# Optimization experiments

Hardware: AMD Instinct MI355X
Metric: run time of the kernel (lower is better)

## Reference

```python
import jax, jax.numpy as jnp
import numpy as np

D_MODEL = 1024
NUM_HEADS = 16
HEAD_DIM = D_MODEL // NUM_HEADS  # 64
ROPE_BASE = 10000.0


def _rope_tables(n_pos, dim):
    # 1D rotary tables for `dim` channels (rotate-half convention).
    inv_freq = 1.0 / (ROPE_BASE ** (jnp.arange(0, dim, 2, dtype=jnp.float32) / dim))
    ang = jnp.arange(n_pos, dtype=jnp.float32)[:, None] * inv_freq[None, :]  # (P, dim/2)
    cos = jnp.concatenate([jnp.cos(ang), jnp.cos(ang)], axis=-1)  # (P, dim)
    sin = jnp.concatenate([jnp.sin(ang), jnp.sin(ang)], axis=-1)
    return cos, sin


def _rotate_half(v):
    v1, v2 = jnp.split(v, 2, axis=-1)
    return jnp.concatenate([-v2, v1], axis=-1)


def rope_2d(x, H, W):
    # x: (N, H, W, nh, hd). First half of hd rotated by row index, second by col index.
    d_half = HEAD_DIM // 2
    x_h, x_w = x[..., :d_half], x[..., d_half:]
    cos_h, sin_h = _rope_tables(H, d_half)  # (H, d_half)
    cos_w, sin_w = _rope_tables(W, d_half)  # (W, d_half)
    cos_h = cos_h[None, :, None, None, :]
    sin_h = sin_h[None, :, None, None, :]
    cos_w = cos_w[None, None, :, None, :]
    sin_w = sin_w[None, None, :, None, :]
    x_h = x_h * cos_h + _rotate_half(x_h) * sin_h
    x_w = x_w * cos_w + _rotate_half(x_w) * sin_w
    return jnp.concatenate([x_h, x_w], axis=-1)


def setup_inputs() -> dict:
    key = jax.random.key(0)
    k_x, k_qkv, k_p, k_b = jax.random.split(key, 4)
    B, T, H, W = 4, 32, 16, 16
    x = jax.random.normal(k_x, (B, T, H, W, D_MODEL), dtype=jnp.float32)
    w_qkv = jax.random.normal(k_qkv, (D_MODEL, 3 * D_MODEL), dtype=jnp.float32) * 0.02
    w_proj = jax.random.normal(k_p, (D_MODEL, D_MODEL), dtype=jnp.float32) * 0.02
    b_proj = jax.random.normal(k_b, (D_MODEL,), dtype=jnp.float32) * 0.02
    return {"x": x, "w_qkv": w_qkv, "w_proj": w_proj, "b_proj": b_proj}


def reference(x, w_qkv, w_proj, b_proj):
    B, T, H, W, C = x.shape
    N, S = B * T, H * W
    scale = HEAD_DIM ** -0.5
    xf = x.reshape(N, S, C)
    qkv = xf @ w_qkv  # (N, S, 3C)  [qkv_bias=False]
    q, k, v = jnp.split(qkv, 3, axis=-1)
    q = q.reshape(N, H, W, NUM_HEADS, HEAD_DIM)
    k = k.reshape(N, H, W, NUM_HEADS, HEAD_DIM)
    v = v.reshape(N, S, NUM_HEADS, HEAD_DIM)
    q = rope_2d(q, H, W).reshape(N, S, NUM_HEADS, HEAD_DIM)
    k = rope_2d(k, H, W).reshape(N, S, NUM_HEADS, HEAD_DIM)
    attn = jnp.einsum('nshd,nthd->nhst', q, k) * scale  # (N, nh, S, S)
    attn = jax.nn.softmax(attn, axis=-1)  # attn_drop=0.0
    out = jnp.einsum('nhst,nthd->nshd', attn, v).reshape(N, S, C)
    out = out @ w_proj + b_proj
    return out.reshape(B, T, H, W, C)
```

## Files before the change

### kernel.cpp

```cpp
#include <hip/hip_runtime.h>
#include <hip/hip_bf16.h>
#include <stdint.h>

typedef __attribute__((ext_vector_type(8))) short bf16x8;
typedef __attribute__((ext_vector_type(4))) float f32x4;
typedef __attribute__((ext_vector_type(4))) unsigned short ushort4_t;

__device__ __forceinline__ unsigned short f2bf(float f) {
  union { float f; unsigned int i; } x; x.f = f;
  return (unsigned short)((x.i + 0x7fffu + ((x.i >> 16) & 1u)) >> 16);
}

__device__ __forceinline__ void gl_lds16(const void* g, void* l) {
  __builtin_amdgcn_global_load_lds(
      (const __attribute__((address_space(1))) unsigned int*)(uintptr_t)g,
      (__attribute__((address_space(3))) unsigned int*)(uint32_t)(uintptr_t)l,
      16, 0, 0);
}

__device__ __forceinline__ void bar() {
  asm volatile("" ::: "memory");
  __builtin_amdgcn_s_barrier();
  asm volatile("" ::: "memory");
}

__constant__ float INVF[16] = {
  1.0f,   0.56234132519f,  0.31622776601f,  0.17782794100f,
  0.1f,   0.056234132519f, 0.031622776601f, 0.017782794100f,
  0.01f,  0.0056234132519f,0.0031622776601f,0.0017782794100f,
  0.001f, 0.00056234132519f,0.00031622776601f,0.00017782794100f
};

__global__ __launch_bounds__(256) void k_conv_x(const float4* __restrict__ src,
                                                ushort4_t* __restrict__ dst, int n4) {
  int i = blockIdx.x * 256 + threadIdx.x;
  if (i < n4) {
    float4 v = src[i];
    ushort4_t r = { f2bf(v.x), f2bf(v.y), f2bf(v.z), f2bf(v.w) };
    dst[i] = r;
  }
}

__global__ __launch_bounds__(256) void k_transpose_bf16(const float* __restrict__ src,
                                                        unsigned short* __restrict__ dst,
                                                        int R, int C) {
  __shared__ unsigned short tile[64][65];
  const int bj = blockIdx.x, bi = blockIdx.y;
  const int t = threadIdx.x, lr = t >> 6, lc = t & 63;
  #pragma unroll
  for (int i = 0; i < 16; i++) {
    int r = i * 4 + lr;
    tile[r][lc] = f2bf(src[(size_t)(bi * 64 + r) * C + bj * 64 + lc]);
  }
  __syncthreads();
  #pragma unroll
  for (int i = 0; i < 16; i++) {
    int r = i * 4 + lr;
    dst[(size_t)(bj * 64 + r) * R + bi * 64 + lc] = tile[lc][r];
  }
}

template<int F32OUT, int ROPE>
__global__ __launch_bounds__(512, 1) void k_gemm_bt(
    const unsigned short* __restrict__ A, const unsigned short* __restrict__ B,
    unsigned short* __restrict__ Cb, float* __restrict__ Cf,
    const float* __restrict__ bias, int M, int N, int K) {
  __shared__ __align__(16) unsigned short As[3 * 256 * 64];
  __shared__ __align__(16) unsigned short Bs[3 * 128 * 64];
  const int tid = threadIdx.x;
  const int lane = tid & 63, wid = tid >> 6;
  const int cl = lane & 15, gr = lane >> 4;
  const int wm = wid >> 1, wn = wid & 1;
  const int l8 = lane >> 3, l7 = lane & 7;
  const int mBase = blockIdx.y * 256, nBase = blockIdx.x * 128;
  const int KT = K >> 6;
  const int ldsW = (wid * 8) * 64;

  const unsigned short* aP[4];
  const unsigned short* bP[2];
  #pragma unroll
  for (int i = 0; i < 4; i++)
    aP[i] = A + (size_t)(mBase + i * 64 + wid * 8 + l8) * K + (l7 ^ l8) * 8;
  #pragma unroll
  for (int i = 0; i < 2; i++)
    bP[i] = B + (size_t)(nBase + i * 64 + wid * 8 + l8) * K + (l7 ^ l8) * 8;

  const f32x4 zero4 = {0.f, 0.f, 0.f, 0.f};
  f32x4 acc[4][4];
  #pragma unroll
  for (int a = 0; a < 4; a++)
    #pragma unroll
    for (int b = 0; b < 4; b++) acc[a][b] = zero4;

  #pragma unroll
  for (int i = 0; i < 4; i++) gl_lds16(aP[i], &As[(i * 64) * 64 + ldsW]);
  #pragma unroll
  for (int i = 0; i < 2; i++) gl_lds16(bP[i], &Bs[(i * 64) * 64 + ldsW]);
  #pragma unroll
  for (int i = 0; i < 4; i++) gl_lds16(aP[i] + 64, &As[16384 + (i * 64) * 64 + ldsW]);
  #pragma unroll
  for (int i = 0; i < 2; i++) gl_lds16(bP[i] + 64, &Bs[8192 + (i * 64) * 64 + ldsW]);
  asm volatile("s_waitcnt vmcnt(6)" ::: "memory");
  bar();

  for (int c = 0; c < KT; ++c) {
    const int s = c % 3;
    const int sn = (c + 2) % 3;
    const unsigned short* as_ = As + s * 16384;
    const unsigned short* bs_ = Bs + s * 8192;
    const bool pf = (c + 2 < KT);

    #pragma unroll
    for (int kc = 0; kc < 2; ++kc) {
      bf16x8 af[4], bfv[4];
      const int coff = ((kc * 4 + gr) ^ (cl & 7)) * 8;
      #pragma unroll
      for (int t = 0; t < 4; t++) {
        af[t]  = *(const bf16x8*)&as_[(wm * 64 + t * 16 + cl) * 64 + coff];
        bfv[t] = *(const bf16x8*)&bs_[(wn * 64 + t * 16 + cl) * 64 + coff];
      }
      if (pf) {
        const int koff = (c + 2) * 64;
        if (kc == 0) {
          gl_lds16(aP[0] + koff, &As[sn * 16384 + (0 * 64) * 64 + ldsW]);
          gl_lds16(aP[1] + koff, &As[sn * 16384 + (1 * 64) * 64 + ldsW]);
          gl_lds16(aP[2] + koff, &As[sn * 16384 + (2 * 64) * 64 + ldsW]);
        } else {
          gl_lds16(aP[3] + koff, &As[sn * 16384 + (3 * 64) * 64 + ldsW]);
          gl_lds16(bP[0] + koff, &Bs[sn * 8192 + (0 * 64) * 64 + ldsW]);
          gl_lds16(bP[1] + koff, &Bs[sn * 8192 + (1 * 64) * 64 + ldsW]);
        }
      }
      bar();
      asm volatile("s_waitcnt lgkmcnt(0)" ::: "memory");
      __builtin_amdgcn_s_setprio(1);
      #pragma unroll
      for (int mt = 0; mt < 4; mt++)
        #pragma unroll
        for (int nt = 0; nt < 4; nt++)
          acc[mt][nt] = __builtin_amdgcn_mfma_f32_16x16x32_bf16(af[mt], bfv[nt], acc[mt][nt], 0, 0, 0);
      __builtin_amdgcn_s_setprio(0);
      if (kc == 0) {
        bar();
      } else {
        if (c + 2 < KT)      asm volatile("s_waitcnt vmcnt(6)" ::: "memory");
        else if (c + 1 < KT) asm volatile("s_waitcnt vmcnt(0)" ::: "memory");
        if (c + 1 < KT) bar();
      }
    }
  }

  if (ROPE && nBase < 2048) {
    const float f = INVF[cl];
    #pragma unroll
    for (int mt = 0; mt < 4; mt++)
      #pragma unroll
      for (int r = 0; r < 4; r++) {
        const int sp = (mBase + wm * 64 + mt * 16 + gr * 4 + r) & 255;
        float sh, ch, sw, cw;
        __sincosf((float)(sp >> 4) * f, &sh, &ch);
        __sincosf((float)(sp & 15) * f, &sw, &cw);
        const float a = acc[mt][0][r], b = acc[mt][1][r];
        const float cc = acc[mt][2][r], d = acc[mt][3][r];
        acc[mt][0][r] = a * ch - b * sh;
        acc[mt][1][r] = b * ch + a * sh;
        acc[mt][2][r] = cc * cw - d * sw;
        acc[mt][3][r] = d * cw + cc * sw;
      }
  }

  #pragma unroll
  for (int mt = 0; mt < 4; mt++)
    #pragma unroll
    for (int nt = 0; nt < 4; nt++)
      #pragma unroll
      for (int r = 0; r < 4; r++) {
        const int row = mBase + wm * 64 + mt * 16 + gr * 4 + r;
        const int col = nBase + wn * 64 + nt * 16 + cl;
        const float v = acc[mt][nt][r];
        if (F32OUT) Cf[(size_t)row * N + col] = v + bias[col];
        else        Cb[(size_t)row * N + col] = f2bf(v);
      }
}

__global__ __launch_bounds__(256, 3) void k_attn(const unsigned short* __restrict__ qkv,
                                                 unsigned short* __restrict__ attn_out) {
  __shared__ __align__(16) unsigned short Qp[4][64 * 64];
  __shared__ __align__(16) unsigned short Kt[64 * 64];
  __shared__ __align__(16) unsigned short Vt[64 * 64];
  const int blk = blockIdx.x;
  const int n = blk >> 4, h = blk & 15;
  const int tid = threadIdx.x;
  const int lane = tid & 63, wid = tid >> 6;
  const int cl = lane & 15, gr = lane >> 4;
  const int l8 = lane >> 3, l7 = lane & 7;
  const unsigned short* qbase = qkv + (size_t)n * 256 * 3072 + h * 64;
  const unsigned short* kbase = qbase + 1024;
  const unsigned short* vbase = qbase + 2048;

  #pragma unroll
  for (int i = 0; i < 8; i++)
    gl_lds16(qbase + (size_t)(wid * 64 + i * 8 + l8) * 3072 + (l7 ^ l8) * 8,
             &Qp[wid][i * 8 * 64]);
  #pragma unroll
  for (int i = 0; i < 2; i++) {
    const int r0 = (wid * 2 + i) * 8;
    gl_lds16(kbase + (size_t)(r0 + l8) * 3072 + (l7 ^ l8) * 8, &Kt[r0 * 64]);
  }

  unsigned int vr[2][4];
  #pragma unroll
  for (int i = 0; i < 2; i++) {
    const int u = i * 256 + tid;
    const int t0 = u >> 5, d = (u & 31) * 2;
    #pragma unroll
    for (int k = 0; k < 4; k++)
      vr[i][k] = *(const unsigned int*)(vbase + (size_t)(t0 + 16 * k) * 3072 + d);
  }
  __syncthreads();

  bf16x8 qf[4][2];
  #pragma unroll
  for (int mt = 0; mt < 4; mt++)
    #pragma unroll
    for (int kc = 0; kc < 2; kc++)
      qf[mt][kc] = *(const bf16x8*)&Qp[wid][(mt * 16 + cl) * 64 + ((kc * 4 + gr) ^ (cl & 7)) * 8];

  const f32x4 zero4 = {0.f, 0.f, 0.f, 0.f};
  f32x4 o[4][4];
  float lsum[4][4];
  #pragma unroll
  for (int a = 0; a < 4; a++)
    #pragma unroll
    for (int b = 0; b < 4; b++) { o[a][b] = zero4; lsum[a][b] = 0.f; }

  for (int tc = 0; tc < 4; tc++) {
    #pragma unroll
    for (int i = 0; i < 2; i++) {
      const int u = i * 256 + tid;
      const int t0 = u >> 5, d = (u & 31) * 2;
      const unsigned int r0 = vr[i][0], r1 = vr[i][1], r2 = vr[i][2], r3 = vr[i][3];
      uint2 lo, hi;
      lo.x = (r0 & 0xffffu) | (r1 << 16);
      lo.y = (r2 & 0xffffu) | (r3 << 16);
      hi.x = (r0 >> 16) | (r1 & 0xffff0000u);
      hi.y = (r2 >> 16) | (r3 & 0xffff0000u);
      *(uint2*)&Vt[d * 64 + ((t0 >> 1) ^ (d & 7)) * 8 + (t0 & 1) * 4] = lo;
      const int d1 = d + 1;
      *(uint2*)&Vt[d1 * 64 + ((t0 >> 1) ^ (d1 & 7)) * 8 + (t0 & 1) * 4] = hi;
    }
    if (tc < 3) {
      #pragma unroll
      for (int i = 0; i < 2; i++) {
        const int u = i * 256 + tid;
        const int t0 = u >> 5, d = (u & 31) * 2;
        #pragma unroll
        for (int k = 0; k < 4; k++)
          vr[i][k] = *(const unsigned int*)(vbase + (size_t)((tc + 1) * 64 + t0 + 16 * k) * 3072 + d);
      }
    }

    #pragma unroll
    for (int mt = 0; mt < 4; mt++) {
      f32x4 sacc[4] = {zero4, zero4, zero4, zero4};
      #pragma unroll
      for (int kc = 0; kc < 2; kc++)
        #pragma unroll
        for (int nt = 0; nt < 4; nt++) {
          const bf16x8 kf = *(const bf16x8*)&Kt[(nt * 16 + cl) * 64 + ((kc * 4 + gr) ^ (cl & 7)) * 8];
          sacc[nt] = __builtin_amdgcn_mfma_f32_16x16x32_bf16(qf[mt][kc], kf, sacc[nt], 0, 0, 0);
        }
      #pragma unroll
      for (int r = 0; r < 4; r++) {
        const float p0 = __expf(sacc[0][r] * 0.125f);
        const float p1 = __expf(sacc[1][r] * 0.125f);
        const float p2 = __expf(sacc[2][r] * 0.125f);
        const float p3 = __expf(sacc[3][r] * 0.125f);
        lsum[mt][r] += (p0 + p1) + (p2 + p3);
        float2 f01; f01.x = p0; f01.y = p1;
        float2 f23; f23.x = p2; f23.y = p3;
        __hip_bfloat162 b01 = __float22bfloat162_rn(f01);
        __hip_bfloat162 b23 = __float22bfloat162_rn(f23);
        union { __hip_bfloat162 h; unsigned int u; } c0, c1;
        c0.h = b01; c1.h = b23;
        uint2 w; w.x = c0.u; w.y = c1.u;
        const int m = mt * 16 + gr * 4 + r;
        *(uint2*)&Qp[wid][m * 64 + ((cl >> 1) ^ (m & 7)) * 8 + (cl & 1) * 4] = w;
      }
    }
    __syncthreads();

    if (tc < 3) {
      #pragma unroll
      for (int i = 0; i < 2; i++) {
        const int r0 = (wid * 2 + i) * 8;
        gl_lds16(kbase + (size_t)((tc + 1) * 64 + r0 + l8) * 3072 + (l7 ^ l8) * 8, &Kt[r0 * 64]);
      }
    }

    #pragma unroll
    for (int kc = 0; kc < 2; kc++) {
      bf16x8 vf[4], pf[4];
      #pragma unroll
      for (int dt = 0; dt < 4; dt++)
        vf[dt] = *(const bf16x8*)&Vt[(dt * 16 + cl) * 64 + ((kc * 4 + gr) ^ (cl & 7)) * 8];
      #pragma unroll
      for (int mt = 0; mt < 4; mt++)
        pf[mt] = *(const bf16x8*)&Qp[wid][(mt * 16 + cl) * 64 + ((kc * 4 + gr) ^ (cl & 7)) * 8];
      #pragma unroll
      for (int mt = 0; mt < 4; mt++)
        #pragma unroll
        for (int dt = 0; dt < 4; dt++)
          o[mt][dt] = __builtin_amdgcn_mfma_f32_16x16x32_bf16(pf[mt], vf[dt], o[mt][dt], 0, 0, 0);
    }
    __syncthreads();
  }

  #pragma unroll
  for (int mt = 0; mt < 4; mt++)
    #pragma unroll
    for (int r = 0; r < 4; r++) {
      float l = lsum[mt][r];
      l += __shfl_xor(l, 1);
      l += __shfl_xor(l, 2);
      l += __shfl_xor(l, 4);
      l += __shfl_xor(l, 8);
      const float inv = 1.0f / l;
      const int srow = wid * 64 + mt * 16 + gr * 4 + r;
      #pragma unroll
      for (int dt = 0; dt < 4; dt++)
        attn_out[(size_t)(n * 256 + srow) * 1024 + h * 64 + dt * 16 + cl] =
            f2bf(o[mt][dt][r] * inv);
    }
}

extern "C" void kernel_launch(void* const* d_in, const int* in_sizes, int n_in,
                              void* d_out, int out_size, void* d_ws, size_t ws_size,
                              hipStream_t stream) {
  const float* x      = (const float*)d_in[0];
  const float* w_qkv  = (const float*)d_in[1];
  const float* w_proj = (const float*)d_in[2];
  const float* b_proj = (const float*)d_in[3];
  float* out = (float*)d_out;
  char* ws = (char*)d_ws;

  unsigned short* x_bf    = (unsigned short*)ws;
  unsigned short* wqkvT   = (unsigned short*)(ws + 67108864);
  unsigned short* wprojT  = (unsigned short*)(ws + 73400320);
  unsigned short* qkvb    = (unsigned short*)(ws + 75497472);
  unsigned short* attn_bf = x_bf;

  k_conv_x<<<32768, 256, 0, stream>>>((const float4*)x, (ushort4_t*)x_bf, 8388608);
  k_transpose_bf16<<<dim3(48, 16), 256, 0, stream>>>(w_qkv, wqkvT, 1024, 3072);
  k_transpose_bf16<<<dim3(16, 16), 256, 0, stream>>>(w_proj, wprojT, 1024, 1024);

  k_gemm_bt<0, 1><<<dim3(24, 128), 512, 0, stream>>>(x_bf, wqkvT, qkvb, nullptr, nullptr,
                                                     32768, 3072, 1024);
  k_attn<<<2048, 256, 0, stream>>>(qkvb, attn_bf);

  k_gemm_bt<1, 0><<<dim3(8, 128), 512, 0, stream>>>(attn_bf, wprojT, nullptr, out, b_proj,
                                                    32768, 1024, 1024);
}
```

Before: 710.0 us.

## Enlarge GEMM tile to 256x256 with double-buffered LDS and 2 blocks/CU

The bf16 GEMM tile grows from 256x128 to 256x256, with a 2x4 warp grid and each warp computing 128x64 (8x4 MFMA tiles). The triple-buffered split prefetch becomes double buffering, where the whole next K-slice is issued at the top of each iteration and waited on once at the end. Launch bounds now ask for 2 blocks per CU. The aim is more arithmetic per LDS/global byte and fewer barriers per K-step. In exchange, the accumulator register count doubles, which may conflict with the 2-block occupancy hint or cause spills, and prefetch overlap is shallower.

Result: faster. 657.2 us (-7.4%).

```diff
diff --git a/kernel.cpp b/kernel.cpp
--- a/kernel.cpp
+++ b/kernel.cpp
@@ -61,123 +61,119 @@
 }
 
 template<int F32OUT, int ROPE>
-__global__ __launch_bounds__(512, 1) void k_gemm_bt(
+__global__ __launch_bounds__(512, 2) void k_gemm_bt(
     const unsigned short* __restrict__ A, const unsigned short* __restrict__ B,
     unsigned short* __restrict__ Cb, float* __restrict__ Cf,
     const float* __restrict__ bias, int M, int N, int K) {
-  __shared__ __align__(16) unsigned short As[3 * 256 * 64];
-  __shared__ __align__(16) unsigned short Bs[3 * 128 * 64];
+  __shared__ __align__(16) unsigned short As[2 * 256 * 64];
+  __shared__ __align__(16) unsigned short Bs[2 * 256 * 64];
   const int tid = threadIdx.x;
   const int lane = tid & 63, wid = tid >> 6;
   const int cl = lane & 15, gr = lane >> 4;
-  const int wm = wid >> 1, wn = wid & 1;
+  const int wm = wid >> 2, wn = wid & 3;
   const int l8 = lane >> 3, l7 = lane & 7;
-  const int mBase = blockIdx.y * 256, nBase = blockIdx.x * 128;
+  const int mBase = blockIdx.y * 256, nBase = blockIdx.x * 256;
   const int KT = K >> 6;
   const int ldsW = (wid * 8) * 64;
 
   const unsigned short* aP[4];
-  const unsigned short* bP[2];
-  #pragma unroll
-  for (int i = 0; i < 4; i++)
+  const unsigned short* bP[4];
+  #pragma unroll
+  for (int i = 0; i < 4; i++) {
     aP[i] = A + (size_t)(mBase + i * 64 + wid * 8 + l8) * K + (l7 ^ l8) * 8;
-  #pragma unroll
-  for (int i = 0; i < 2; i++)
     bP[i] = B + (size_t)(nBase + i * 64 + wid * 8 + l8) * K + (l7 ^ l8) * 8;
+  }
 
   const f32x4 zero4 = {0.f, 0.f, 0.f, 0.f};
-  f32x4 acc[4][4];
-  #pragma unroll
-  for (int a = 0; a < 4; a++)
+  f32x4 acc[8][4];
+  #pragma unroll
+  for (int a = 0; a < 8; a++)
     #pragma unroll
     for (int b = 0; b < 4; b++) acc[a][b] = zero4;
 
   #pragma unroll
   for (int i = 0; i < 4; i++) gl_lds16(aP[i], &As[(i * 64) * 64 + ldsW]);
   #pragma unroll
-  for (int i = 0; i < 2; i++) gl_lds16(bP[i], &Bs[(i * 64) * 64 + ldsW]);
+  for (int i = 0; i < 4; i++) gl_lds16(bP[i], &Bs[(i * 64) * 64 + ldsW]);
   #pragma unroll
   for (int i = 0; i < 4; i++) gl_lds16(aP[i] + 64, &As[16384 + (i * 64) * 64 + ldsW]);
   #pragma unroll
-  for (int i = 0; i < 2; i++) gl_lds16(bP[i] + 64, &Bs[8192 + (i * 64) * 64 + ldsW]);
-  asm volatile("s_waitcnt vmcnt(6)" ::: "memory");
+  for (int i = 0; i < 4; i++) gl_lds16(bP[i] + 64, &Bs[16384 + (i * 64) * 64 + ldsW]);
+  asm volatile("s_waitcnt vmcnt(8)" ::: "memory");
   bar();
 
   for (int c = 0; c < KT; ++c) {
-    const int s = c % 3;
-    const int sn = (c + 2) % 3;
+    const int s = c & 1;
     const unsigned short* as_ = As + s * 16384;
-    const unsigned short* bs_ = Bs + s * 8192;
-    const bool pf = (c + 2 < KT);
+    const unsigned short* bs_ = Bs + s * 16384;
+
+    if (c + 1 < KT) {
+      const int koff = (c + 1) * 64;
+      const int so = (s ^ 1) * 16384;
+      #pragma unroll
+      for (int i = 0; i < 4; i++) gl_lds16(aP[i] + koff, &As[so + (i * 64) * 64 + ldsW]);
+      #pragma unroll
+      for (int i = 0; i < 4; i++) gl_lds16(bP[i] + koff, &Bs[so + (i * 64) * 64 + ldsW]);
+    }
 
     #pragma unroll
     for (int kc = 0; kc < 2; ++kc) {
-      bf16x8 af[4], bfv[4];
       const int coff = ((kc * 4 + gr) ^ (cl & 7)) * 8;
-      #pragma unroll
-      for (int t = 0; t < 4; t++) {
-        af[t]  = *(const bf16x8*)&as_[(wm * 64 + t * 16 + cl) * 64 + coff];
-        bfv[t] = *(const bf16x8*)&bs_[(wn * 64 + t * 16 + cl) * 64 + coff];
-      }
-      if (pf) {
-        const int koff = (c + 2) * 64;
-        if (kc == 0) {
-          gl_lds16(aP[0] + koff, &As[sn * 16384 + (0 * 64) * 64 + ldsW]);
-          gl_lds16(aP[1] + koff, &As[sn * 16384 + (1 * 64) * 64 + ldsW]);
-          gl_lds16(aP[2] + koff, &As[sn * 16384 + (2 * 64) * 64 + ldsW]);
-        } else {
-          gl_lds16(aP[3] + koff, &As[sn * 16384 + (3 * 64) * 64 + ldsW]);
-          gl_lds16(bP[0] + koff, &Bs[sn * 8192 + (0 * 64) * 64 + ldsW]);
-          gl_lds16(bP[1] + koff, &Bs[sn * 8192 + (1 * 64) * 64 + ldsW]);
-        }
-      }
+      bf16x8 bv[4];
+      #pragma unroll
+      for (int nt = 0; nt < 4; nt++)
+        bv[nt] = *(const bf16x8*)&bs_[(wn * 64 + nt * 16 + cl) * 64 + coff];
+      #pragma unroll
+      for (int h = 0; h < 2; ++h) {
+        bf16x8 af[4];
+        #pragma unroll
+        for (int t = 0; t < 4; t++)
+          af[t] = *(const bf16x8*)&as_[(wm * 128 + h * 64 + t * 16 + cl) * 64 + coff];
+        __builtin_amdgcn_s_setprio(1);
+        #pragma unroll
+        for (int mt = 0; mt < 4; mt++)
+          #pragma unroll
+          for (int nt = 0; nt < 4; nt++)
+            acc[h * 4 + mt][nt] =
+                __builtin_amdgcn_mfma_f32_16x16x32_bf16(af[mt], bv[nt], acc[h * 4 + mt][nt], 0, 0, 0);
+        __builtin_amdgcn_s_setprio(0);
+      }
+    }
+
+    if (c + 1 < KT) {
+      asm volatile("s_waitcnt vmcnt(0)" ::: "memory");
       bar();
-      asm volatile("s_waitcnt lgkmcnt(0)" ::: "memory");
-      __builtin_amdgcn_s_setprio(1);
-      #pragma unroll
-      for (int mt = 0; mt < 4; mt++)
-        #pragma unroll
-        for (int nt = 0; nt < 4; nt++)
-          acc[mt][nt] = __builtin_amdgcn_mfma_f32_16x16x32_bf16(af[mt], bfv[nt], acc[mt][nt], 0, 0, 0);
-      __builtin_amdgcn_s_setprio(0);
-      if (kc == 0) {
-        bar();
-      } else {
-        if (c + 2 < KT)      asm volatile("s_waitcnt vmcnt(6)" ::: "memory");
-        else if (c + 1 < KT) asm volatile("s_waitcnt vmcnt(0)" ::: "memory");
-        if (c + 1 < KT) bar();
-      }
     }
   }
 
   if (ROPE && nBase < 2048) {
     const float f = INVF[cl];
     #pragma unroll
-    for (int mt = 0; mt < 4; mt++)
+    for (int amt = 0; amt < 8; amt++)
       #pragma unroll
       for (int r = 0; r < 4; r++) {
-        const int sp = (mBase + wm * 64 + mt * 16 + gr * 4 + r) & 255;
+        const int sp = (mBase + wm * 128 + amt * 16 + gr * 4 + r) & 255;
         float sh, ch, sw, cw;
         __sincosf((float)(sp >> 4) * f, &sh, &ch);
         __sincosf((float)(sp & 15) * f, &sw, &cw);
-        const float a = acc[mt][0][r], b = acc[mt][1][r];
-        const float cc = acc[mt][2][r], d = acc[mt][3][r];
-        acc[mt][0][r] = a * ch - b * sh;
-        acc[mt][1][r] = b * ch + a * sh;
-        acc[mt][2][r] = cc * cw - d * sw;
-        acc[mt][3][r] = d * cw + cc * sw;
-      }
-  }
-
-  #pragma unroll
-  for (int mt = 0; mt < 4; mt++)
+        const float a = acc[amt][0][r], b = acc[amt][1][r];
+        const float cc = acc[amt][2][r], d = acc[amt][3][r];
+        acc[amt][0][r] = a * ch - b * sh;
+        acc[amt][1][r] = b * ch + a * sh;
+        acc[amt][2][r] = cc * cw - d * sw;
+        acc[amt][3][r] = d * cw + cc * sw;
+      }
+  }
+
+  #pragma unroll
+  for (int amt = 0; amt < 8; amt++)
     #pragma unroll
     for (int nt = 0; nt < 4; nt++)
       #pragma unroll
       for (int r = 0; r < 4; r++) {
-        const int row = mBase + wm * 64 + mt * 16 + gr * 4 + r;
+        const int row = mBase + wm * 128 + amt * 16 + gr * 4 + r;
         const int col = nBase + wn * 64 + nt * 16 + cl;
-        const float v = acc[mt][nt][r];
+        const float v = acc[amt][nt][r];
         if (F32OUT) Cf[(size_t)row * N + col] = v + bias[col];
         else        Cb[(size_t)row * N + col] = f2bf(v);
       }
@@ -354,10 +350,10 @@
   k_transpose_bf16<<<dim3(48, 16), 256, 0, stream>>>(w_qkv, wqkvT, 1024, 3072);
   k_transpose_bf16<<<dim3(16, 16), 256, 0, stream>>>(w_proj, wprojT, 1024, 1024);
 
-  k_gemm_bt<0, 1><<<dim3(24, 128), 512, 0, stream>>>(x_bf, wqkvT, qkvb, nullptr, nullptr,
+  k_gemm_bt<0, 1><<<dim3(12, 128), 512, 0, stream>>>(x_bf, wqkvT, qkvb, nullptr, nullptr,
                                                      32768, 3072, 1024);
   k_attn<<<2048, 256, 0, stream>>>(qkvb, attn_bf);
 
-  k_gemm_bt<1, 0><<<dim3(8, 128), 512, 0, stream>>>(attn_bf, wprojT, nullptr, out, b_proj,
+  k_gemm_bt<1, 0><<<dim3(4, 128), 512, 0, stream>>>(attn_bf, wprojT, nullptr, out, b_proj,
                                                     32768, 1024, 1024);
 }
```
